# Performance work log

Measured on AMD Instinct MI355X. Metric: run time of the kernel, lower is better.

Reference implementation:

```python
import jax, jax.numpy as jnp
import numpy as np

ORDER = 2  # diffusion steps per support
NUM_LAYERS = 2


def gconv(z, supports, W, b):
    # z: [B,N,C]; supports: [S,N,N]; concat [z, S1 z, S1^2 z, S2 z, S2^2 z] -> dense proj
    feats = [z]
    for si in range(supports.shape[0]):
        s = supports[si]
        zk = z
        for _ in range(ORDER):
            zk = jnp.einsum('mn,bnc->bmc', s, zk)
            feats.append(zk)
    zcat = jnp.concatenate(feats, axis=-1)  # [B,N,C*(1+S*ORDER)]
    return zcat @ W + b


def dcgru_cell(x, h, supports, Wg, bg, Wc, bc):
    H = h.shape[-1]
    zr = jax.nn.sigmoid(gconv(jnp.concatenate([x, h], axis=-1), supports, Wg, bg))
    z, r = zr[..., :H], zr[..., H:]
    hc = jnp.tanh(gconv(jnp.concatenate([x, r * h], axis=-1), supports, Wc, bc))
    return z * h + (1.0 - z) * hc


def setup_inputs() -> dict:
    key = jax.random.key(0)
    ks = jax.random.split(key, 32)
    B, T, N, D_IN, H = 64, 12, 325, 2, 128
    K = 1 + 2 * ORDER  # 5 diffusion matrices
    inp = {}
    inp['source'] = jax.random.normal(ks[0], (B, T, N, D_IN), jnp.float32)
    inp['targets'] = jax.random.normal(ks[1], (B, T, N, D_IN), jnp.float32)
    u = jax.random.uniform(ks[2], (2, N, N), jnp.float32)
    inp['supports'] = u / jnp.sum(u, axis=-1, keepdims=True)  # row-stochastic random walks
    sc = 0.05
    inp['enc_Wg0'] = sc * jax.random.normal(ks[3], ((D_IN + H) * K, 2 * H), jnp.float32)
    inp['enc_bg0'] = jnp.zeros((2 * H,), jnp.float32)
    inp['enc_Wc0'] = sc * jax.random.normal(ks[4], ((D_IN + H) * K, H), jnp.float32)
    inp['enc_bc0'] = jnp.zeros((H,), jnp.float32)
    inp['enc_Wg1'] = sc * jax.random.normal(ks[5], ((H + H) * K, 2 * H), jnp.float32)
    inp['enc_bg1'] = jnp.zeros((2 * H,), jnp.float32)
    inp['enc_Wc1'] = sc * jax.random.normal(ks[6], ((H + H) * K, H), jnp.float32)
    inp['enc_bc1'] = jnp.zeros((H,), jnp.float32)
    inp['dec_Wg0'] = sc * jax.random.normal(ks[7], ((D_IN + H) * K, 2 * H), jnp.float32)
    inp['dec_bg0'] = jnp.zeros((2 * H,), jnp.float32)
    inp['dec_Wc0'] = sc * jax.random.normal(ks[8], ((D_IN + H) * K, H), jnp.float32)
    inp['dec_bc0'] = jnp.zeros((H,), jnp.float32)
    inp['dec_Wg1'] = sc * jax.random.normal(ks[9], ((H + H) * K, 2 * H), jnp.float32)
    inp['dec_bg1'] = jnp.zeros((2 * H,), jnp.float32)
    inp['dec_Wc1'] = sc * jax.random.normal(ks[10], ((H + H) * K, H), jnp.float32)
    inp['dec_bc1'] = jnp.zeros((H,), jnp.float32)
    inp['Wp'] = sc * jax.random.normal(ks[11], (H, D_IN), jnp.float32)
    inp['bp'] = jnp.zeros((D_IN,), jnp.float32)
    return inp


def _forward(source, targets, supports,
             enc_Wg0, enc_bg0, enc_Wc0, enc_bc0, enc_Wg1, enc_bg1, enc_Wc1, enc_bc1,
             dec_Wg0, dec_bg0, dec_Wc0, dec_bc0, dec_Wg1, dec_bg1, dec_Wc1, dec_bc1,
             Wp, bp):
    B, T_in, N, D_in = source.shape
    T_out = targets.shape[1]
    enc_params = [(enc_Wg0, enc_bg0, enc_Wc0, enc_bc0), (enc_Wg1, enc_bg1, enc_Wc1, enc_bc1)]
    dec_params = [(dec_Wg0, dec_bg0, dec_Wc0, dec_bc0), (dec_Wg1, dec_bg1, dec_Wc1, dec_bc1)]

    # ---- encoder: per layer, scan over time ----
    cur = jnp.swapaxes(source, 0, 1)  # [T,B,N,C]
    enc_finals = []
    for (Wg, bg, Wc, bc) in enc_params:
        H = Wc.shape[-1]
        h0 = jnp.zeros((B, N, H), source.dtype)
        def step(h, xt, Wg=Wg, bg=bg, Wc=Wc, bc=bc):
            h2 = dcgru_cell(xt, h, supports, Wg, bg, Wc, bc)
            return h2, h2
        hT, hs = jax.lax.scan(step, h0, cur)
        enc_finals.append(hT)
        cur = hs

    # ---- decoder (teacher_forcing_ratio = 0 for determinism) ----
    out_dim = Wp.shape[-1]
    go = jnp.zeros((B, N, out_dim), source.dtype)  # GO symbol

    def dec_step(carry, _):
        states, cur_in = carry
        new_states = []
        x = cur_in
        for i, (Wg, bg, Wc, bc) in enumerate(dec_params):
            s = dcgru_cell(x, states[i], supports, Wg, bg, Wc, bc)
            x = s
            new_states.append(s)
        out = jnp.einsum('bnh,ho->bno', x, Wp) + bp  # [B,N,out_dim]
        return (tuple(new_states), out), out

    _, outs = jax.lax.scan(dec_step, (tuple(enc_finals), go), None, length=T_out)
    return jnp.swapaxes(outs, 0, 1)  # [B,T_out,N,out_dim]


def reference(source, targets, supports,
              enc_Wg0, enc_bg0, enc_Wc0, enc_bc0, enc_Wg1, enc_bg1, enc_Wc1, enc_bc1,
              dec_Wg0, dec_bg0, dec_Wc0, dec_bc0, dec_Wg1, dec_bg1, dec_Wc1, dec_bc1,
              Wp, bp):
    return _forward(source, targets, supports,
                    enc_Wg0, enc_bg0, enc_Wc0, enc_bc0, enc_Wg1, enc_bg1, enc_Wc1, enc_bc1,
                    dec_Wg0, dec_bg0, dec_Wc0, dec_bc0, dec_Wg1, dec_bg1, dec_Wc1, dec_bc1,
                    Wp, bp)
```

## Files before the change

### kernel.cpp

```cpp
#include <hip/hip_runtime.h>
#include <hip/hip_bf16.h>

#define B_  64
#define T_  12
#define N_  325
#define DIN 2
#define H_  128
#define BN  (B_*N_)
#define DPITCH 384
#define AROWS 384

typedef __hip_bfloat16 bf16;
typedef unsigned short u16;
typedef __attribute__((ext_vector_type(8))) short short8;
typedef __attribute__((ext_vector_type(4))) float f32x4;

__device__ __forceinline__ float b2f(bf16 v){ return __bfloat162float(v); }
__device__ __forceinline__ u16 f2b(float f){
    __hip_bfloat16 h = __float2bfloat16(f);
    return *reinterpret_cast<u16*>(&h);
}
__device__ __forceinline__ float ldf(const void* p, size_t i, int bf){
    return bf ? b2f(((const bf16*)p)[i]) : ((const float*)p)[i];
}

__device__ __forceinline__ void gl_lds16(const u16* g, u16* l){
    __builtin_amdgcn_global_load_lds(
        (const __attribute__((address_space(1))) unsigned int*)g,
        (__attribute__((address_space(3))) unsigned int*)l, 16, 0, 0);
}

struct FillCfg { u16 *F, *Ft; const float *x, *h; long xbs; int C, KC, Cpad, Din, b0, nb; };
struct DiffCfg { u16* F; const u16* Ft; int C, KC, Cpad, coff, ctiles, T, nb; };
struct GemmCfg { const u16* Fb; const u16* Wt; const float* bias; float* zr; float* hb;
                 int KC, KCpad, rows, gy, ct, nb; };
struct RhCfg  { u16 *F, *Ft; const float *zr, *h; int KC, Cpad, Din, b0, total, nb; };

__global__ void sniff(const void* __restrict__ sup, int* __restrict__ flag){
    if (threadIdx.x == 0 && blockIdx.x == 0){
        float sb = 0.f, sf = 0.f;
        for (int n = 0; n < N_; ++n){
            sb += b2f(((const bf16*)sup)[n]);
            sf += ((const float*)sup)[n];
        }
        float db = fabsf(sb - 1.f), df = fabsf(sf - 1.f);
        *flag = (db < df) ? 1 : 0;
    }
}

struct CvtArgs { const void* src[12]; float* dst[12]; int n[12]; };

__global__ void cvt_all(CvtArgs a, const int* __restrict__ flag){
    int ii = blockIdx.y;
    int i  = blockIdx.x*256 + threadIdx.x;
    if (i >= a.n[ii]) return;
    a.dst[ii][i] = ldf(a.src[ii], i, *flag);
}

__global__ void support_prep(const void* __restrict__ sup, const int* __restrict__ flag,
                             float* __restrict__ msq){
    int bf = *flag;
    int s = blockIdx.z;
    int m = blockIdx.y*16 + threadIdx.y;
    int n = blockIdx.x*16 + threadIdx.x;
    __shared__ float As[16][17], Bs[16][17];
    size_t base = (size_t)s*N_*N_;
    float acc = 0.f;
    for (int j0 = 0; j0 < N_; j0 += 16){
        As[threadIdx.y][threadIdx.x] = (m < N_ && j0+threadIdx.x < N_) ? ldf(sup, base + (size_t)m*N_ + j0+threadIdx.x, bf) : 0.f;
        Bs[threadIdx.y][threadIdx.x] = (j0+threadIdx.y < N_ && n < N_) ? ldf(sup, base + (size_t)(j0+threadIdx.y)*N_ + n, bf) : 0.f;
        __syncthreads();
        #pragma unroll
        for (int jj=0; jj<16; ++jj) acc += As[threadIdx.y][jj]*Bs[jj][threadIdx.x];
        __syncthreads();
    }
    if (m < N_ && n < N_){
        msq[(size_t)(2*s  )*N_*N_ + m*N_ + n] = ldf(sup, base + (size_t)m*N_ + n, bf);
        msq[(size_t)(2*s+1)*N_*N_ + m*N_ + n] = acc;
    }
}

__global__ void asq_prep(const float* __restrict__ msq, u16* __restrict__ asq){
    int idx = blockIdx.x*256 + threadIdx.x;
    int total = 4*AROWS*DPITCH;
    if (idx >= total) return;
    int col = idx % DPITCH;
    int rm  = idx / DPITCH;
    int m   = rm % AROWS;
    int k   = rm / AROWS;
    asq[idx] = (m < N_ && col < N_) ? f2b(msq[((size_t)k*N_ + m)*N_ + col]) : 0;
}

__global__ __launch_bounds__(256) void wtrans(const void* __restrict__ W, u16* __restrict__ Wt,
                                              int KC, int Nout, int KCpad,
                                              const int* __restrict__ flag){
    int bf = *flag;
    int k0 = blockIdx.x*64, c0 = blockIdx.y*64;
    int tid = threadIdx.x;
    __shared__ u16 T[64][72];
    #pragma unroll
    for (int it=0; it<2; ++it){
        int lin = it*256 + tid;
        int kl = lin >> 3, seg = lin & 7;
        int gk = k0 + kl, gc = c0 + seg*8;
        u16 tmp[8];
        #pragma unroll
        for (int e=0;e<8;++e) tmp[e] = (gk < KC) ? f2b(ldf(W, (size_t)gk*Nout + gc + e, bf)) : 0;
        *(uint4*)&T[kl][seg*8] = *(const uint4*)tmp;
    }
    __syncthreads();
    #pragma unroll
    for (int it=0; it<2; ++it){
        int lin = it*256 + tid;
        int cl = lin >> 3, seg = lin & 7;
        u16 tmp[8];
        #pragma unroll
        for (int j=0;j<8;++j) tmp[j] = T[seg*8+j][cl];
        *(uint4*)(Wt + (size_t)(c0+cl)*KCpad + k0 + seg*8) = *(const uint4*)tmp;
    }
}

__global__ __launch_bounds__(256) void fill_k(FillCfg ca, FillCfg cb, int na){
    int bi = blockIdx.x;
    FillCfg c = ca;
    if (bi >= na){ c = cb; bi -= na; }
    int gyc  = c.Cpad >> 6;
    int nblk = bi % 6;
    int rest = bi / 6;
    int cblk = rest % gyc;
    int bl   = rest / gyc;
    int bg = c.b0 + bl;
    int n0 = nblk*64, c0 = cblk*64;
    int tid = threadIdx.x;
    __shared__ u16 T[64][72];
    #pragma unroll
    for (int it=0; it<2; ++it){
        int lin = it*256 + tid;
        int nl = lin >> 3, seg = lin & 7;
        int gn = n0 + nl;
        u16 tmp[8];
        #pragma unroll
        for (int e=0;e<8;++e){
            int cc = c0 + seg*8 + e;
            float v = 0.f;
            if (gn < N_ && cc < c.C)
                v = (cc < c.Din) ? c.x[(size_t)bg*c.xbs + (size_t)gn*c.Din + cc]
                                 : c.h[((size_t)bg*N_ + gn)*H_ + (cc - c.Din)];
            tmp[e] = f2b(v);
        }
        *(uint4*)&T[nl][seg*8] = *(const uint4*)tmp;
        if (gn < N_){
            int cbase = c0 + seg*8;
            u16* dst = c.F + ((size_t)bl*N_ + gn)*c.KC + cbase;
            if (cbase + 7 < c.C){
                *(uint4*)dst = *(const uint4*)tmp;
            } else {
                #pragma unroll
                for (int e=0;e<8;++e) if (cbase + e < c.C) dst[e] = tmp[e];
            }
        }
    }
    __syncthreads();
    #pragma unroll
    for (int it=0; it<2; ++it){
        int lin = it*256 + tid;
        int cl = lin >> 3, seg = lin & 7;
        u16 tmp[8];
        #pragma unroll
        for (int j=0;j<8;++j) tmp[j] = T[seg*8+j][cl];
        *(uint4*)(c.Ft + (size_t)bl*c.Cpad*DPITCH + (size_t)(c0+cl)*DPITCH + n0 + seg*8)
            = *(const uint4*)tmp;
    }
}

__global__ void rh_k(RhCfg ca, RhCfg cb, int na){
    int blk = blockIdx.x;
    RhCfg c = ca;
    if (blk >= na){ c = cb; blk -= na; }
    int idx = blk*256 + threadIdx.x;
    if (idx >= c.total) return;
    int j   = idx & 127;
    int bnl = idx >> 7;
    int bl  = bnl / N_;
    int n   = bnl % N_;
    float r  = c.zr[(size_t)bnl*256 + 128 + j];
    float hv = c.h[((size_t)c.b0*N_ + bnl)*128 + j];
    u16 v = f2b(r * hv);
    c.F[(size_t)bnl*c.KC + c.Din + j] = v;
    c.Ft[((size_t)bl*c.Cpad + c.Din + j)*DPITCH + n] = v;
}

__global__ __launch_bounds__(256) void diffuse_k(DiffCfg ca, DiffCfg cb, int na,
                                                 const u16* __restrict__ asq){
    int bi = blockIdx.x;
    DiffCfg c = ca;
    if (bi >= na){ c = cb; bi -= na; }
    int xcd = bi & 7, m8 = bi >> 3;
    int tg = m8 / 12, s = m8 % 12;
    int t = tg*8 + xcd;
    if (t >= c.T) return;
    int bl = t / c.ctiles, cbk = t % c.ctiles;
    int y = s % 3, k = s / 3;

    const u16* A    = asq + (size_t)k*AROWS*DPITCH;
    const u16* Bt_g = c.Ft + ((size_t)bl*c.Cpad + c.coff)*DPITCH;
    u16*       Cm   = c.F + (size_t)bl*N_*c.KC + (size_t)(k+1)*c.C + c.coff;

    int m0 = y * 128;
    int c0 = cbk * 64;
    int tid = threadIdx.x;
    int wv = tid >> 6, lane = tid & 63, l15 = lane & 15, quad = lane >> 4;
    int lr = lane >> 3, ls = lane & 7;

    __shared__ u16 As[128*64];
    __shared__ u16 Bs[64*64];

    f32x4 acc[2][4];
    #pragma unroll
    for (int i2=0;i2<2;++i2)
        #pragma unroll
        for (int j=0;j<4;++j) acc[i2][j] = (f32x4){0.f,0.f,0.f,0.f};

    for (int k0 = 0; k0 < N_; k0 += 64){
        #pragma unroll
        for (int j=0;j<4;++j){
            int row = wv*32 + j*8 + lr;
            int seg = ls ^ lr;
            gl_lds16(A + (size_t)(m0+row)*DPITCH + k0 + seg*8, &As[(wv*32 + j*8)*64]);
        }
        #pragma unroll
        for (int j=0;j<2;++j){
            int row = wv*16 + j*8 + lr;
            int seg = ls ^ lr;
            gl_lds16(Bt_g + (size_t)(c0+row)*DPITCH + k0 + seg*8, &Bs[(wv*16 + j*8)*64]);
        }
        __syncthreads();
        #pragma unroll
        for (int ks = 0; ks < 64; ks += 32){
            int sw = (((ks>>3) + quad) ^ (l15 & 7)) << 3;
            short8 a0 = *(const short8*)&As[(wv*32      + l15)*64 + sw];
            short8 a1 = *(const short8*)&As[(wv*32 + 16 + l15)*64 + sw];
            short8 b0 = *(const short8*)&Bs[(     l15)*64 + sw];
            short8 b1 = *(const short8*)&Bs[(16 + l15)*64 + sw];
            short8 b2 = *(const short8*)&Bs[(32 + l15)*64 + sw];
            short8 b3 = *(const short8*)&Bs[(48 + l15)*64 + sw];
            acc[0][0] = __builtin_amdgcn_mfma_f32_16x16x32_bf16(a0,b0,acc[0][0],0,0,0);
            acc[0][1] = __builtin_amdgcn_mfma_f32_16x16x32_bf16(a0,b1,acc[0][1],0,0,0);
            acc[0][2] = __builtin_amdgcn_mfma_f32_16x16x32_bf16(a0,b2,acc[0][2],0,0,0);
            acc[0][3] = __builtin_amdgcn_mfma_f32_16x16x32_bf16(a0,b3,acc[0][3],0,0,0);
            acc[1][0] = __builtin_amdgcn_mfma_f32_16x16x32_bf16(a1,b0,acc[1][0],0,0,0);
            acc[1][1] = __builtin_amdgcn_mfma_f32_16x16x32_bf16(a1,b1,acc[1][1],0,0,0);
            acc[1][2] = __builtin_amdgcn_mfma_f32_16x16x32_bf16(a1,b2,acc[1][2],0,0,0);
            acc[1][3] = __builtin_amdgcn_mfma_f32_16x16x32_bf16(a1,b3,acc[1][3],0,0,0);
        }
        __syncthreads();
    }
    #pragma unroll
    for (int i2=0;i2<2;++i2){
        #pragma unroll
        for (int j=0;j<4;++j){
            int cc = c0 + j*16 + l15;
            #pragma unroll
            for (int r=0;r<4;++r){
                int m = m0 + wv*32 + i2*16 + quad*4 + r;
                if (m < N_ && c.coff + cc < c.C) Cm[(size_t)m*c.KC + cc] = f2b(acc[i2][j][r]);
            }
        }
    }
}

template<int MODE>
__global__ __launch_bounds__(256) void gemm_k(GemmCfg ca, GemmCfg cb, int na){
    int bi = blockIdx.x;
    GemmCfg c = ca;
    if (bi >= na){ c = cb; bi -= na; }
    int xcd = bi & 7, q = bi >> 3;
    int cbk = q % c.ct;
    int rt  = (q / c.ct)*8 + xcd;
    if (rt >= c.gy) return;
    int r0 = rt * 128;
    int c0 = cbk * 64;
    int tid = threadIdx.x;
    int wv = tid >> 6, lane = tid & 63, l15 = lane & 15, quad = lane >> 4;
    int lr = lane >> 3, ls = lane & 7;

    __shared__ u16 As[128*64];
    __shared__ u16 Bs[64*64];

    f32x4 acc[2][4];
    #pragma unroll
    for (int i2=0;i2<2;++i2)
        #pragma unroll
        for (int j=0;j<4;++j) acc[i2][j] = (f32x4){0.f,0.f,0.f,0.f};

    for (int k0 = 0; k0 < c.KCpad; k0 += 64){
        if (k0 + 64 <= c.KC){
            #pragma unroll
            for (int j=0;j<4;++j){
                int row = wv*32 + j*8 + lr;
                int seg = ls ^ lr;
                gl_lds16(c.Fb + (size_t)(r0+row)*c.KC + k0 + seg*8, &As[(wv*32 + j*8)*64]);
            }
        } else {
            #pragma unroll
            for (int it=0; it<4; ++it){
                int lin = it*256 + tid;
                int row = lin >> 3, sp = lin & 7;
                int seg = sp ^ (row & 7);
                int gr = r0 + row, gk = k0 + seg*8;
                u16 tmp[8];
                #pragma unroll
                for (int e=0;e<8;++e)
                    tmp[e] = (gk+e < c.KC) ? c.Fb[(size_t)gr*c.KC + gk+e] : (u16)0;
                *(uint4*)&As[row*64 + sp*8] = *(const uint4*)tmp;
            }
        }
        #pragma unroll
        for (int j=0;j<2;++j){
            int row = wv*16 + j*8 + lr;
            int seg = ls ^ lr;
            gl_lds16(c.Wt + (size_t)(c0+row)*c.KCpad + k0 + seg*8, &Bs[(wv*16 + j*8)*64]);
        }
        __syncthreads();
        #pragma unroll
        for (int ks = 0; ks < 64; ks += 32){
            int sw = (((ks>>3) + quad) ^ (l15 & 7)) << 3;
            short8 a0 = *(const short8*)&As[(wv*32      + l15)*64 + sw];
            short8 a1 = *(const short8*)&As[(wv*32 + 16 + l15)*64 + sw];
            short8 b0 = *(const short8*)&Bs[(     l15)*64 + sw];
            short8 b1 = *(const short8*)&Bs[(16 + l15)*64 + sw];
            short8 b2 = *(const short8*)&Bs[(32 + l15)*64 + sw];
            short8 b3 = *(const short8*)&Bs[(48 + l15)*64 + sw];
            acc[0][0] = __builtin_amdgcn_mfma_f32_16x16x32_bf16(a0,b0,acc[0][0],0,0,0);
            acc[0][1] = __builtin_amdgcn_mfma_f32_16x16x32_bf16(a0,b1,acc[0][1],0,0,0);
            acc[0][2] = __builtin_amdgcn_mfma_f32_16x16x32_bf16(a0,b2,acc[0][2],0,0,0);
            acc[0][3] = __builtin_amdgcn_mfma_f32_16x16x32_bf16(a0,b3,acc[0][3],0,0,0);
            acc[1][0] = __builtin_amdgcn_mfma_f32_16x16x32_bf16(a1,b0,acc[1][0],0,0,0);
            acc[1][1] = __builtin_amdgcn_mfma_f32_16x16x32_bf16(a1,b1,acc[1][1],0,0,0);
            acc[1][2] = __builtin_amdgcn_mfma_f32_16x16x32_bf16(a1,b2,acc[1][2],0,0,0);
            acc[1][3] = __builtin_amdgcn_mfma_f32_16x16x32_bf16(a1,b3,acc[1][3],0,0,0);
        }
        __syncthreads();
    }
    #pragma unroll
    for (int i2=0;i2<2;++i2){
        #pragma unroll
        for (int j=0;j<4;++j){
            int cc = c0 + j*16 + l15;
            #pragma unroll
            for (int r=0;r<4;++r){
                int gr = r0 + wv*32 + i2*16 + quad*4 + r;
                if (gr >= c.rows) continue;
                float v = acc[i2][j][r] + c.bias[cc];
                if (MODE == 0){
                    v = 1.f/(1.f + __expf(-v));
                    c.zr[(size_t)gr*256 + cc] = v;
                } else {
                    float hc   = tanhf(v);
                    float z    = c.zr[(size_t)gr*256 + cc];
                    float hold = c.hb[(size_t)gr*128 + cc];
                    c.hb[(size_t)gr*128 + cc] = z*hold + (1.f - z)*hc;
                }
            }
        }
    }
}

__global__ __launch_bounds__(256) void proj(const float* __restrict__ h1,
                                            const float* __restrict__ Wp,
                                            const float* __restrict__ bp,
                                            float* __restrict__ xdec,
                                            float* __restrict__ out, int t){
    int row  = blockIdx.x * 4 + (threadIdx.x >> 6);
    int lane = threadIdx.x & 63;
    float v0 = h1[(size_t)row*128 + lane];
    float v1 = h1[(size_t)row*128 + 64 + lane];
    float w00 = Wp[lane*2+0],      w01 = Wp[lane*2+1];
    float w10 = Wp[(64+lane)*2+0], w11 = Wp[(64+lane)*2+1];
    float a0 = v0*w00 + v1*w10;
    float a1 = v0*w01 + v1*w11;
    #pragma unroll
    for (int off=32; off>0; off>>=1){
        a0 += __shfl_down(a0, off);
        a1 += __shfl_down(a1, off);
    }
    if (lane == 0){
        a0 += bp[0];
        a1 += bp[1];
        xdec[(size_t)row*2+0] = a0;
        xdec[(size_t)row*2+1] = a1;
        int b = row / N_, n = row % N_;
        size_t o = ((size_t)(b*T_ + t)*N_ + n)*2;
        out[o]   = a0;
        out[o+1] = a1;
    }
}

struct Layer {
    u16 *F, *Ft; float *zr; float *h;
    const u16 *Wg, *Wc; const float *bg, *bc;
    int C, KC, KCpad, Din, ctiles, Cpad;
};

extern "C" void kernel_launch(void* const* d_in, const int* in_sizes, int n_in,
                              void* d_out, int out_size, void* d_ws, size_t ws_size,
                              hipStream_t stream){
    float* out = (float*)d_out;

    char* pb = (char*)d_ws;
    auto alloc = [&](size_t bytes)->void*{
        void* r = (void*)pb;
        pb += (bytes + 255) & ~(size_t)255;
        return r;
    };

    int* flag = (int*)alloc(16);
    sniff<<<1, 64, 0, stream>>>(d_in[2], flag);

    const int idxs[11] = {0,4,6,8,10,12,14,16,18,19,20};
    float* cw[21] = {nullptr};
    CvtArgs ca;
    int maxn = 0;
    for (int ii = 0; ii < 11; ++ii){
        int i = idxs[ii];
        int n = in_sizes[i];
        cw[i] = (float*)alloc((size_t)n*4);
        ca.src[ii] = d_in[i];
        ca.dst[ii] = cw[i];
        ca.n[ii]   = n;
        if (n > maxn) maxn = n;
    }
    cvt_all<<<dim3((maxn+255)/256, 11), 256, 0, stream>>>(ca, flag);
    const float* src = cw[0];

    float* msq  = (float*)alloc((size_t)4*N_*N_*4);
    float* h0   = (float*)alloc((size_t)BN*H_*4);
    float* h1   = (float*)alloc((size_t)BN*H_*4);
    float* xdec = (float*)alloc((size_t)BN*DIN*4);
    u16*   asq  = (u16*)alloc((size_t)4*AROWS*DPITCH*2);

    const int widx[8]  = {3,5,7,9,11,13,15,17};
    const int wKC[8]   = {650,650,1280,1280,650,650,1280,1280};
    const int wNout[8] = {256,128,256,128,256,128,256,128};
    u16* wt[8];
    for (int i=0;i<8;++i){
        int KCpad = (wKC[i] + 63) & ~63;
        wt[i] = (u16*)alloc((size_t)wNout[i]*KCpad*2);
        wtrans<<<dim3(KCpad/64, wNout[i]/64), 256, 0, stream>>>(d_in[widx[i]], wt[i], wKC[i], wNout[i], KCpad, flag);
    }

    {
        dim3 g((N_+15)/16, (N_+15)/16, 2), b(16,16);
        support_prep<<<g, b, 0, stream>>>(d_in[2], flag, msq);
        int tot = 4*AROWS*DPITCH;
        asq_prep<<<dim3((tot+255)/256), 256, 0, stream>>>(msq, asq);
    }
    hipMemsetAsync(h0, 0, sizeof(float)*(size_t)BN*H_*2, stream);

    size_t fixed = (size_t)(pb - (char*)d_ws);
    size_t need0 = (size_t)BN*256*4 + (size_t)BN*650*2  + (size_t)B_*192*DPITCH*2;
    size_t need1 = (size_t)BN*256*4 + (size_t)BN*1280*2 + (size_t)B_*256*DPITCH*2;
    bool dual = (fixed + need0 + need1 + (4<<20)) <= ws_size;

    auto mkFill = [&](Layer& L, const float* x, long xbs, int b0, int Bc)->FillCfg{
        return FillCfg{L.F, L.Ft, x, L.h, xbs, L.C, L.KC, L.Cpad, L.Din, b0,
                       6*(L.Cpad/64)*Bc};
    };
    auto mkD1 = [&](Layer& L, int Bc)->DiffCfg{
        int T = Bc*L.ctiles;
        return DiffCfg{L.F, L.Ft, L.C, L.KC, L.Cpad, 0, L.ctiles, T, 12*(((T+7)/8)*8)};
    };
    auto mkD2 = [&](Layer& L, int Bc)->DiffCfg{
        int T = Bc*2;
        return DiffCfg{L.F, L.Ft, L.C, L.KC, L.Cpad, L.Din, 2, T, 12*(((T+7)/8)*8)};
    };
    auto mkG0 = [&](Layer& L, int b0, int Bc)->GemmCfg{
        int rows = Bc*N_, gy = (rows+127)/128;
        return GemmCfg{L.F, L.Wg, L.bg, L.zr, L.h + (size_t)b0*N_*H_,
                       L.KC, L.KCpad, rows, gy, 4, 8*((gy+7)/8)*4};
    };
    auto mkG1 = [&](Layer& L, int b0, int Bc)->GemmCfg{
        int rows = Bc*N_, gy = (rows+127)/128;
        return GemmCfg{L.F, L.Wc, L.bc, L.zr, L.h + (size_t)b0*N_*H_,
                       L.KC, L.KCpad, rows, gy, 2, 8*((gy+7)/8)*2};
    };
    auto mkRh = [&](Layer& L, int b0, int Bc)->RhCfg{
        int total = Bc*N_*H_;
        return RhCfg{L.F, L.Ft, L.zr, L.h, L.KC, L.Cpad, L.Din, b0, total, (total+255)/256};
    };
    auto runCellSeq = [&](Layer& L, const float* x, long xbs, int b0, int Bc){
        FillCfg f = mkFill(L, x, xbs, b0, Bc);
        fill_k<<<dim3(f.nb), 256, 0, stream>>>(f, f, f.nb);
        DiffCfg d1 = mkD1(L, Bc);
        diffuse_k<<<dim3(d1.nb), 256, 0, stream>>>(d1, d1, d1.nb, asq);
        GemmCfg g0 = mkG0(L, b0, Bc);
        gemm_k<0><<<dim3(g0.nb), 256, 0, stream>>>(g0, g0, g0.nb);
        RhCfg r = mkRh(L, b0, Bc);
        rh_k<<<dim3(r.nb), 256, 0, stream>>>(r, r, r.nb);
        DiffCfg d2 = mkD2(L, Bc);
        diffuse_k<<<dim3(d2.nb), 256, 0, stream>>>(d2, d2, d2.nb, asq);
        GemmCfg g1 = mkG1(L, b0, Bc);
        gemm_k<1><<<dim3(g1.nb), 256, 0, stream>>>(g1, g1, g1.nb);
    };

    if (dual){
        float* zr0 = (float*)alloc((size_t)BN*256*4);
        u16*   F0  = (u16*)alloc((size_t)BN*650*2);
        u16*   Ft0 = (u16*)alloc((size_t)B_*192*DPITCH*2);
        float* zr1 = (float*)alloc((size_t)BN*256*4);
        u16*   F1  = (u16*)alloc((size_t)BN*1280*2);
        u16*   Ft1 = (u16*)alloc((size_t)B_*256*DPITCH*2);
        alloc(1<<19);

        Layer E0{F0, Ft0, zr0, h0, wt[0], wt[1], cw[4],  cw[6],  130, 650, 704, 2,   3, 192};
        Layer E1{F1, Ft1, zr1, h1, wt[2], wt[3], cw[8],  cw[10], 256, 1280,1280,128, 4, 256};
        Layer D0{F0, Ft0, zr0, h0, wt[4], wt[5], cw[12], cw[14], 130, 650, 704, 2,   3, 192};
        Layer D1{F1, Ft1, zr1, h1, wt[6], wt[7], cw[16], cw[18], 256, 1280,1280,128, 4, 256};

        for (int s = 0; s <= T_; ++s){
            bool has0 = (s < T_), has1 = (s >= 1);
            const float* x0 = src + (size_t)s*N_*DIN;
            FillCfg f0 = mkFill(E0, x0, (long)T_*N_*DIN, 0, B_);
            FillCfg f1 = mkFill(E1, h0, (long)N_*H_,     0, B_);
            if (has0 && has1) fill_k<<<dim3(f0.nb+f1.nb),256,0,stream>>>(f0, f1, f0.nb);
            else if (has0)    fill_k<<<dim3(f0.nb),256,0,stream>>>(f0, f0, f0.nb);
            else              fill_k<<<dim3(f1.nb),256,0,stream>>>(f1, f1, f1.nb);

            DiffCfg a1 = mkD1(E0, B_), b1 = mkD1(E1, B_);
            if (has0 && has1) diffuse_k<<<dim3(a1.nb+b1.nb),256,0,stream>>>(a1, b1, a1.nb, asq);
            else if (has0)    diffuse_k<<<dim3(a1.nb),256,0,stream>>>(a1, a1, a1.nb, asq);
            else              diffuse_k<<<dim3(b1.nb),256,0,stream>>>(b1, b1, b1.nb, asq);

            GemmCfg ga = mkG0(E0, 0, B_), gb = mkG0(E1, 0, B_);
            if (has0 && has1) gemm_k<0><<<dim3(ga.nb+gb.nb),256,0,stream>>>(ga, gb, ga.nb);
            else if (has0)    gemm_k<0><<<dim3(ga.nb),256,0,stream>>>(ga, ga, ga.nb);
            else              gemm_k<0><<<dim3(gb.nb),256,0,stream>>>(gb, gb, gb.nb);

            RhCfg ra = mkRh(E0, 0, B_), rb = mkRh(E1, 0, B_);
            if (has0 && has1) rh_k<<<dim3(ra.nb+rb.nb),256,0,stream>>>(ra, rb, ra.nb);
            else if (has0)    rh_k<<<dim3(ra.nb),256,0,stream>>>(ra, ra, ra.nb);
            else              rh_k<<<dim3(rb.nb),256,0,stream>>>(rb, rb, rb.nb);

            DiffCfg a2 = mkD2(E0, B_), b2 = mkD2(E1, B_);
            if (has0 && has1) diffuse_k<<<dim3(a2.nb+b2.nb),256,0,stream>>>(a2, b2, a2.nb, asq);
            else if (has0)    diffuse_k<<<dim3(a2.nb),256,0,stream>>>(a2, a2, a2.nb, asq);
            else              diffuse_k<<<dim3(b2.nb),256,0,stream>>>(b2, b2, b2.nb, asq);

            GemmCfg ha = mkG1(E0, 0, B_), hb = mkG1(E1, 0, B_);
            if (has0 && has1) gemm_k<1><<<dim3(ha.nb+hb.nb),256,0,stream>>>(ha, hb, ha.nb);
            else if (has0)    gemm_k<1><<<dim3(ha.nb),256,0,stream>>>(ha, ha, ha.nb);
            else              gemm_k<1><<<dim3(hb.nb),256,0,stream>>>(hb, hb, hb.nb);
        }

        hipMemsetAsync(xdec, 0, sizeof(float)*(size_t)BN*DIN, stream);
        for (int t = 0; t < T_; ++t){
            runCellSeq(D0, xdec, (long)N_*DIN, 0, B_);
            runCellSeq(D1, h0,   (long)N_*H_,  0, B_);
            proj<<<dim3(BN/4), 256, 0, stream>>>(h1, cw[19], cw[20], xdec, out, t);
        }
    } else {
        size_t perb = (size_t)N_*1280*2 + (size_t)N_*256*4 + (size_t)256*DPITCH*2;
        int Bc = 64;
        while (Bc > 2 && fixed + (1<<20) + (size_t)Bc*perb > ws_size) Bc >>= 1;
        float* zr = (float*)alloc((size_t)Bc*N_*256*4);
        u16*   F  = (u16*)alloc((size_t)Bc*N_*1280*2);
        u16*   Ft = (u16*)alloc((size_t)Bc*256*DPITCH*2);
        alloc(1<<19);

        Layer SE0{F, Ft, zr, h0, wt[0], wt[1], cw[4],  cw[6],  130, 650, 704, 2,   3, 192};
        Layer SE1{F, Ft, zr, h1, wt[2], wt[3], cw[8],  cw[10], 256, 1280,1280,128, 4, 256};
        Layer SD0{F, Ft, zr, h0, wt[4], wt[5], cw[12], cw[14], 130, 650, 704, 2,   3, 192};
        Layer SD1{F, Ft, zr, h1, wt[6], wt[7], cw[16], cw[18], 256, 1280,1280,128, 4, 256};

        for (int t = 0; t < T_; ++t){
            for (int b0 = 0; b0 < B_; b0 += Bc)
                runCellSeq(SE0, src + (size_t)t*N_*DIN, (long)T_*N_*DIN, b0, Bc);
            for (int b0 = 0; b0 < B_; b0 += Bc)
                runCellSeq(SE1, h0, (long)N_*H_, b0, Bc);
        }
        hipMemsetAsync(xdec, 0, sizeof(float)*(size_t)BN*DIN, stream);
        for (int t = 0; t < T_; ++t){
            for (int b0 = 0; b0 < B_; b0 += Bc)
                runCellSeq(SD0, xdec, (long)N_*DIN, b0, Bc);
            for (int b0 = 0; b0 < B_; b0 += Bc)
                runCellSeq(SD1, h0, (long)N_*H_, b0, Bc);
            proj<<<dim3(BN/4), 256, 0, stream>>>(h1, cw[19], cw[20], xdec, out, t);
        }
    }
}
```

Measured before the change: 6.053 ms.

## Pack transposed features densely and replace scalar r*h kernel with tiled transpose

For the first layer, the transposed feature buffer shrinks from a 192-channel to a 130-channel pitch. The diffusion kernel now tiles over a flattened batch-channel index, and its tiles can straddle batch boundaries, so no MFMA work is spent on padding channels. The per-element r*h kernel, which did strided scattered stores into the transposed buffer, is replaced by a 64x64 LDS-tiled kernel that writes both layouts with vector stores. Epilogue index logic gets more complex, with a wrap check per column.

```diff
diff --git a/kernel.cpp b/kernel.cpp
--- a/kernel.cpp
+++ b/kernel.cpp
@@ -31,10 +31,10 @@
 }
 
 struct FillCfg { u16 *F, *Ft; const float *x, *h; long xbs; int C, KC, Cpad, Din, b0, nb; };
-struct DiffCfg { u16* F; const u16* Ft; int C, KC, Cpad, coff, ctiles, T, nb; };
+struct DiffCfg { u16* F; const u16* Ft; int C, KC, Cpad, coff0, tpb, T, fcmax, nb; };
 struct GemmCfg { const u16* Fb; const u16* Wt; const float* bias; float* zr; float* hb;
                  int KC, KCpad, rows, gy, ct, nb; };
-struct RhCfg  { u16 *F, *Ft; const float *zr, *h; int KC, Cpad, Din, b0, total, nb; };
+struct RhCfg  { u16 *F, *Ft; const float *zr, *h; int KC, Cpad, Din, b0, nb; };
 
 __global__ void sniff(const void* __restrict__ sup, int* __restrict__ flag){
     if (threadIdx.x == 0 && blockIdx.x == 0){
@@ -124,7 +124,7 @@
     int bi = blockIdx.x;
     FillCfg c = ca;
     if (bi >= na){ c = cb; bi -= na; }
-    int gyc  = c.Cpad >> 6;
+    int gyc  = (c.C + 63) >> 6;
     int nblk = bi % 6;
     int rest = bi / 6;
     int cblk = rest % gyc;
@@ -165,29 +165,68 @@
     for (int it=0; it<2; ++it){
         int lin = it*256 + tid;
         int cl = lin >> 3, seg = lin & 7;
+        if (c0 + cl < c.C){
+            u16 tmp[8];
+            #pragma unroll
+            for (int j=0;j<8;++j) tmp[j] = T[seg*8+j][cl];
+            *(uint4*)(c.Ft + ((size_t)bl*c.Cpad + (size_t)(c0+cl))*DPITCH + n0 + seg*8)
+                = *(const uint4*)tmp;
+        }
+    }
+}
+
+__global__ __launch_bounds__(256) void rhfill_k(RhCfg ca, RhCfg cb, int na){
+    int bi = blockIdx.x;
+    RhCfg c = ca;
+    if (bi >= na){ c = cb; bi -= na; }
+    int nblk = bi % 6;
+    int rest = bi / 6;
+    int cblk = rest & 1;
+    int bl   = rest >> 1;
+    int bg = c.b0 + bl;
+    int n0 = nblk*64, ch0 = cblk*64;
+    int tid = threadIdx.x;
+    __shared__ u16 T[64][72];
+    #pragma unroll
+    for (int it=0; it<2; ++it){
+        int lin = it*256 + tid;
+        int nl = lin >> 3, seg = lin & 7;
+        int gn = n0 + nl;
         u16 tmp[8];
+        if (gn < N_){
+            size_t rloc = (size_t)bl*N_ + gn;
+            size_t rg   = (size_t)bg*N_ + gn;
+            const float* zp = c.zr + rloc*256 + 128 + ch0 + seg*8;
+            const float* hp = c.h  + rg*128 + ch0 + seg*8;
+            float4 z0 = *(const float4*)zp, z1 = *(const float4*)(zp+4);
+            float4 h0 = *(const float4*)hp, h1 = *(const float4*)(hp+4);
+            tmp[0]=f2b(z0.x*h0.x); tmp[1]=f2b(z0.y*h0.y);
+            tmp[2]=f2b(z0.z*h0.z); tmp[3]=f2b(z0.w*h0.w);
+            tmp[4]=f2b(z1.x*h1.x); tmp[5]=f2b(z1.y*h1.y);
+            tmp[6]=f2b(z1.z*h1.z); tmp[7]=f2b(z1.w*h1.w);
+            u16* fp = c.F + rloc*c.KC + c.Din + ch0 + seg*8;
+            #pragma unroll
+            for (int e=0;e<4;++e){
+                unsigned w = (unsigned)tmp[2*e] | ((unsigned)tmp[2*e+1] << 16);
+                *(unsigned*)(fp + 2*e) = w;
+            }
+        } else {
+            #pragma unroll
+            for (int e=0;e<8;++e) tmp[e] = 0;
+        }
+        *(uint4*)&T[nl][seg*8] = *(const uint4*)tmp;
+    }
+    __syncthreads();
+    #pragma unroll
+    for (int it=0; it<2; ++it){
+        int lin = it*256 + tid;
+        int cl = lin >> 3, seg = lin & 7;
+        u16 tmp[8];
         #pragma unroll
         for (int j=0;j<8;++j) tmp[j] = T[seg*8+j][cl];
-        *(uint4*)(c.Ft + (size_t)bl*c.Cpad*DPITCH + (size_t)(c0+cl)*DPITCH + n0 + seg*8)
-            = *(const uint4*)tmp;
-    }
-}
-
-__global__ void rh_k(RhCfg ca, RhCfg cb, int na){
-    int blk = blockIdx.x;
-    RhCfg c = ca;
-    if (blk >= na){ c = cb; blk -= na; }
-    int idx = blk*256 + threadIdx.x;
-    if (idx >= c.total) return;
-    int j   = idx & 127;
-    int bnl = idx >> 7;
-    int bl  = bnl / N_;
-    int n   = bnl % N_;
-    float r  = c.zr[(size_t)bnl*256 + 128 + j];
-    float hv = c.h[((size_t)c.b0*N_ + bnl)*128 + j];
-    u16 v = f2b(r * hv);
-    c.F[(size_t)bnl*c.KC + c.Din + j] = v;
-    c.Ft[((size_t)bl*c.Cpad + c.Din + j)*DPITCH + n] = v;
+        size_t row = (size_t)bl*c.Cpad + c.Din + ch0 + cl;
+        *(uint4*)(c.Ft + row*DPITCH + n0 + seg*8) = *(const uint4*)tmp;
+    }
 }
 
 __global__ __launch_bounds__(256) void diffuse_k(DiffCfg ca, DiffCfg cb, int na,
@@ -199,15 +238,21 @@
     int tg = m8 / 12, s = m8 % 12;
     int t = tg*8 + xcd;
     if (t >= c.T) return;
-    int bl = t / c.ctiles, cbk = t % c.ctiles;
     int y = s % 3, k = s / 3;
+    int fc0;
+    if (c.tpb){
+        int blb = t / c.tpb, tb = t - blb*c.tpb;
+        fc0 = blb*c.Cpad + c.coff0 + tb*64;
+    } else {
+        fc0 = t*64;
+    }
+    int bl0  = fc0 / c.Cpad;
+    int rem0 = fc0 - bl0*c.Cpad;
 
     const u16* A    = asq + (size_t)k*AROWS*DPITCH;
-    const u16* Bt_g = c.Ft + ((size_t)bl*c.Cpad + c.coff)*DPITCH;
-    u16*       Cm   = c.F + (size_t)bl*N_*c.KC + (size_t)(k+1)*c.C + c.coff;
+    const u16* Bt_g = c.Ft + (size_t)fc0*DPITCH;
 
     int m0 = y * 128;
-    int c0 = cbk * 64;
     int tid = threadIdx.x;
     int wv = tid >> 6, lane = tid & 63, l15 = lane & 15, quad = lane >> 4;
     int lr = lane >> 3, ls = lane & 7;
@@ -232,7 +277,7 @@
         for (int j=0;j<2;++j){
             int row = wv*16 + j*8 + lr;
             int seg = ls ^ lr;
-            gl_lds16(Bt_g + (size_t)(c0+row)*DPITCH + k0 + seg*8, &Bs[(wv*16 + j*8)*64]);
+            gl_lds16(Bt_g + (size_t)row*DPITCH + k0 + seg*8, &Bs[(wv*16 + j*8)*64]);
         }
         __syncthreads();
         #pragma unroll
@@ -256,14 +301,20 @@
         __syncthreads();
     }
     #pragma unroll
-    for (int i2=0;i2<2;++i2){
-        #pragma unroll
-        for (int j=0;j<4;++j){
-            int cc = c0 + j*16 + l15;
+    for (int j=0;j<4;++j){
+        int d  = j*16 + l15;
+        int cr = rem0 + d;
+        int wrap = (cr >= c.Cpad) ? 1 : 0;
+        int bl = bl0 + wrap;
+        int cc = wrap ? (cr - c.Cpad) : cr;
+        int ok = (fc0 + d) < c.fcmax;
+        u16* Cm = c.F + (size_t)bl*N_*c.KC + (size_t)(k+1)*c.C + cc;
+        #pragma unroll
+        for (int i2=0;i2<2;++i2){
             #pragma unroll
             for (int r=0;r<4;++r){
                 int m = m0 + wv*32 + i2*16 + quad*4 + r;
-                if (m < N_ && c.coff + cc < c.C) Cm[(size_t)m*c.KC + cc] = f2b(acc[i2][j][r]);
+                if (ok && m < N_) Cm[(size_t)m*c.KC] = f2b(acc[i2][j][r]);
             }
         }
     }
@@ -399,7 +450,7 @@
 struct Layer {
     u16 *F, *Ft; float *zr; float *h;
     const u16 *Wg, *Wc; const float *bg, *bc;
-    int C, KC, KCpad, Din, ctiles, Cpad;
+    int C, KC, KCpad, Din, Cpad;
 };
 
 extern "C" void kernel_launch(void* const* d_in, const int* in_sizes, int n_in,
@@ -458,21 +509,24 @@
     hipMemsetAsync(h0, 0, sizeof(float)*(size_t)BN*H_*2, stream);
 
     size_t fixed = (size_t)(pb - (char*)d_ws);
-    size_t need0 = (size_t)BN*256*4 + (size_t)BN*650*2  + (size_t)B_*192*DPITCH*2;
+    size_t need0 = (size_t)BN*256*4 + (size_t)BN*650*2  + (size_t)B_*130*DPITCH*2;
     size_t need1 = (size_t)BN*256*4 + (size_t)BN*1280*2 + (size_t)B_*256*DPITCH*2;
     bool dual = (fixed + need0 + need1 + (4<<20)) <= ws_size;
 
     auto mkFill = [&](Layer& L, const float* x, long xbs, int b0, int Bc)->FillCfg{
         return FillCfg{L.F, L.Ft, x, L.h, xbs, L.C, L.KC, L.Cpad, L.Din, b0,
-                       6*(L.Cpad/64)*Bc};
+                       6*((L.C+63)>>6)*Bc};
     };
     auto mkD1 = [&](Layer& L, int Bc)->DiffCfg{
-        int T = Bc*L.ctiles;
-        return DiffCfg{L.F, L.Ft, L.C, L.KC, L.Cpad, 0, L.ctiles, T, 12*(((T+7)/8)*8)};
+        int fcmax = Bc*L.Cpad;
+        int T = fcmax >> 6;
+        return DiffCfg{L.F, L.Ft, L.C, L.KC, L.Cpad, 0, 0, T, fcmax,
+                       12*(((T+7)/8)*8)};
     };
     auto mkD2 = [&](Layer& L, int Bc)->DiffCfg{
         int T = Bc*2;
-        return DiffCfg{L.F, L.Ft, L.C, L.KC, L.Cpad, L.Din, 2, T, 12*(((T+7)/8)*8)};
+        return DiffCfg{L.F, L.Ft, L.C, L.KC, L.Cpad, L.Din, 2, T, Bc*L.Cpad,
+                       12*(((T+7)/8)*8)};
     };
     auto mkG0 = [&](Layer& L, int b0, int Bc)->GemmCfg{
         int rows = Bc*N_, gy = (rows+127)/128;
@@ -485,8 +539,7 @@
                        L.KC, L.KCpad, rows, gy, 2, 8*((gy+7)/8)*2};
     };
     auto mkRh = [&](Layer& L, int b0, int Bc)->RhCfg{
-        int total = Bc*N_*H_;
-        return RhCfg{L.F, L.Ft, L.zr, L.h, L.KC, L.Cpad, L.Din, b0, total, (total+255)/256};
+        return RhCfg{L.F, L.Ft, L.zr, L.h, L.KC, L.Cpad, L.Din, b0, 12*Bc};
     };
     auto runCellSeq = [&](Layer& L, const float* x, long xbs, int b0, int Bc){
         FillCfg f = mkFill(L, x, xbs, b0, Bc);
@@ -496,7 +549,7 @@
         GemmCfg g0 = mkG0(L, b0, Bc);
         gemm_k<0><<<dim3(g0.nb), 256, 0, stream>>>(g0, g0, g0.nb);
         RhCfg r = mkRh(L, b0, Bc);
-        rh_k<<<dim3(r.nb), 256, 0, stream>>>(r, r, r.nb);
+        rhfill_k<<<dim3(r.nb), 256, 0, stream>>>(r, r, r.nb);
         DiffCfg d2 = mkD2(L, Bc);
         diffuse_k<<<dim3(d2.nb), 256, 0, stream>>>(d2, d2, d2.nb, asq);
         GemmCfg g1 = mkG1(L, b0, Bc);
@@ -506,16 +559,16 @@
     if (dual){
         float* zr0 = (float*)alloc((size_t)BN*256*4);
         u16*   F0  = (u16*)alloc((size_t)BN*650*2);
-        u16*   Ft0 = (u16*)alloc((size_t)B_*192*DPITCH*2);
+        u16*   Ft0 = (u16*)alloc((size_t)B_*130*DPITCH*2);
         float* zr1 = (float*)alloc((size_t)BN*256*4);
         u16*   F1  = (u16*)alloc((size_t)BN*1280*2);
         u16*   Ft1 = (u16*)alloc((size_t)B_*256*DPITCH*2);
         alloc(1<<19);
 
-        Layer E0{F0, Ft0, zr0, h0, wt[0], wt[1], cw[4],  cw[6],  130, 650, 704, 2,   3, 192};
-        Layer E1{F1, Ft1, zr1, h1, wt[2], wt[3], cw[8],  cw[10], 256, 1280,1280,128, 4, 256};
-        Layer D0{F0, Ft0, zr0, h0, wt[4], wt[5], cw[12], cw[14], 130, 650, 704, 2,   3, 192};
-        Layer D1{F1, Ft1, zr1, h1, wt[6], wt[7], cw[16], cw[18], 256, 1280,1280,128, 4, 256};
+        Layer E0{F0, Ft0, zr0, h0, wt[0], wt[1], cw[4],  cw[6],  130, 650, 704, 2,   130};
+        Layer E1{F1, Ft1, zr1, h1, wt[2], wt[3], cw[8],  cw[10], 256, 1280,1280,128, 256};
+        Layer D0{F0, Ft0, zr0, h0, wt[4], wt[5], cw[12], cw[14], 130, 650, 704, 2,   130};
+        Layer D1{F1, Ft1, zr1, h1, wt[6], wt[7], cw[16], cw[18], 256, 1280,1280,128, 256};
 
         for (int s = 0; s <= T_; ++s){
             bool has0 = (s < T_), has1 = (s >= 1);
@@ -537,9 +590,9 @@
             else              gemm_k<0><<<dim3(gb.nb),256,0,stream>>>(gb, gb, gb.nb);
 
             RhCfg ra = mkRh(E0, 0, B_), rb = mkRh(E1, 0, B_);
-            if (has0 && has1) rh_k<<<dim3(ra.nb+rb.nb),256,0,stream>>>(ra, rb, ra.nb);
-            else if (has0)    rh_k<<<dim3(ra.nb),256,0,stream>>>(ra, ra, ra.nb);
-            else              rh_k<<<dim3(rb.nb),256,0,stream>>>(rb, rb, rb.nb);
+            if (has0 && has1) rhfill_k<<<dim3(ra.nb+rb.nb),256,0,stream>>>(ra, rb, ra.nb);
+            else if (has0)    rhfill_k<<<dim3(ra.nb),256,0,stream>>>(ra, ra, ra.nb);
+            else              rhfill_k<<<dim3(rb.nb),256,0,stream>>>(rb, rb, rb.nb);
 
             DiffCfg a2 = mkD2(E0, B_), b2 = mkD2(E1, B_);
             if (has0 && has1) diffuse_k<<<dim3(a2.nb+b2.nb),256,0,stream>>>(a2, b2, a2.nb, asq);
@@ -567,10 +620,10 @@
         u16*   Ft = (u16*)alloc((size_t)Bc*256*DPITCH*2);
         alloc(1<<19);
 
-        Layer SE0{F, Ft, zr, h0, wt[0], wt[1], cw[4],  cw[6],  130, 650, 704, 2,   3, 192};
-        Layer SE1{F, Ft, zr, h1, wt[2], wt[3], cw[8],  cw[10], 256, 1280,1280,128, 4, 256};
-        Layer SD0{F, Ft, zr, h0, wt[4], wt[5], cw[12], cw[14], 130, 650, 704, 2,   3, 192};
-        Layer SD1{F, Ft, zr, h1, wt[6], wt[7], cw[16], cw[18], 256, 1280,1280,128, 4, 256};
+        Layer SE0{F, Ft, zr, h0, wt[0], wt[1], cw[4],  cw[6],  130, 650, 704, 2,   130};
+        Layer SE1{F, Ft, zr, h1, wt[2], wt[3], cw[8],  cw[10], 256, 1280,1280,128, 256};
+        Layer SD0{F, Ft, zr, h0, wt[4], wt[5], cw[12], cw[14], 130, 650, 704, 2,   130};
+        Layer SD1{F, Ft, zr, h1, wt[6], wt[7], cw[16], cw[18], 256, 1280,1280,128, 256};
 
         for (int t = 0; t < T_; ++t){
             for (int b0 = 0; b0 < B_; b0 += Bc)
```

Result: faster. 5.402 ms (-10.8%).
